# Optimization experiments

Measured on AMD Instinct MI355X. Metric: run time of the kernel, lower is better.

The kernel has to match this reference:

```python
import jax, jax.numpy as jnp
import numpy as np

ROT_DELTA = 1  # rotation_delta from __init__
BN_EPS = 1e-3  # keras BatchNormalization default epsilon


def conv_dirac(signal, bc_idx, bc_w, W, b):
    """Template-based intrinsic mesh conv (dirac patch operator).

    signal: [N, D]; bc_idx/bc_w: [N, Rr, A, 3]; W: [T, Rr, A, D]; b: [T].
    Returns [N, K, T] with K = A // ROT_DELTA rotations.
    """
    gathered = signal[bc_idx]  # [N, Rr, A, 3, D] irregular gather
    interp = jnp.einsum('vrai,vraid->vrad', bc_w, gathered)  # barycentric interp
    A = interp.shape[2]
    rots = np.arange(0, A, ROT_DELTA)
    # Rotating the (small) template weights is equivalent to rolling the
    # interpolated signal along the angular axis, but far cheaper.
    W_rot = jnp.stack([jnp.roll(W, int(r), axis=2) for r in rots])  # [K, T, Rr, A, D]
    return jnp.einsum('vrad,ktrad->vkt', interp, W_rot) + b  # [N, K, T]


def angular_max_pool(x):
    # Select, per vertex, the rotation whose response has maximal L2 norm.
    k = jnp.argmax(jnp.linalg.norm(x, axis=-1), axis=1)  # [N]
    return jnp.take_along_axis(x, k[:, None, None], axis=1)[:, 0]  # [N, T]


def batch_norm(x, gamma, beta):
    mu = jnp.mean(x, axis=0, keepdims=True)
    var = jnp.var(x, axis=0, keepdims=True)
    return gamma * (x - mu) * jax.lax.rsqrt(var + BN_EPS) + beta


def setup_inputs() -> dict:
    key = jax.random.key(0)
    ks = jax.random.split(key, 6)
    N, Rr, A, D, T = 80000, 5, 8, 32, 32
    signal = jax.random.normal(ks[0], (N, D), dtype=jnp.float32)
    bc_idx = jax.random.randint(ks[1], (N, Rr, A, 3), 0, N)
    bc_w = jax.random.uniform(ks[2], (N, Rr, A, 3), dtype=jnp.float32)
    bc_w = bc_w / jnp.sum(bc_w, axis=-1, keepdims=True)  # barycentric coords sum to 1
    W1 = jax.random.normal(ks[3], (T, Rr, A, D), dtype=jnp.float32) * 0.05
    W2 = jax.random.normal(ks[4], (T, Rr, A, D), dtype=jnp.float32) * 0.05
    return {
        'signal': signal, 'bc_idx': bc_idx, 'bc_w': bc_w,
        'W1': W1, 'b1': jnp.zeros((T,), jnp.float32),
        'gamma1': jnp.ones((T,), jnp.float32), 'beta1': jnp.zeros((T,), jnp.float32),
        'W2': W2, 'b2': jnp.zeros((T,), jnp.float32),
        'gamma2': jnp.ones((T,), jnp.float32), 'beta2': jnp.zeros((T,), jnp.float32),
    }


def reference(signal, bc_idx, bc_w, W1, b1, gamma1, beta1, W2, b2, gamma2, beta2):
    # Branch 1: conv -> angular max-pool -> BN -> relu
    s = conv_dirac(signal, bc_idx, bc_w, W1, b1)
    s = angular_max_pool(s)
    s = batch_norm(s, gamma1, beta1)
    s = jax.nn.relu(s)
    # Branch 2: conv -> angular max-pool -> BN
    s = conv_dirac(s, bc_idx, bc_w, W2, b2)
    s = angular_max_pool(s)
    s = batch_norm(s, gamma2, beta2)
    # Residual add (input_dim == amt_templates -> no rescale branch) + activation
    return jax.nn.relu(s + signal)
```

## Files before the change

kernel.cpp:

```cpp
#include <hip/hip_runtime.h>
#include <math.h>

#define RR 5
#define AA 8
#define DD 32
#define TT 32
#define KK 8

#define RT2 0.70710678118654752f

typedef float v2f __attribute__((ext_vector_type(2)));
typedef float v4f __attribute__((ext_vector_type(4)));

static __device__ __forceinline__ v2f pkfma(v2f a, v2f b, v2f c) {
#if __has_builtin(__builtin_elementwise_fma)
    return __builtin_elementwise_fma(a, b, c);
#else
    v2f r; r.x = fmaf(a.x, b.x, c.x); r.y = fmaf(a.y, b.y, c.y); return r;
#endif
}
static __device__ __forceinline__ v4f pkfma4(v4f a, v4f b, v4f c) {
#if __has_builtin(__builtin_elementwise_fma)
    return __builtin_elementwise_fma(a, b, c);
#else
    v4f r;
    r.x = fmaf(a.x, b.x, c.x); r.y = fmaf(a.y, b.y, c.y);
    r.z = fmaf(a.z, b.z, c.z); r.w = fmaf(a.w, b.w, c.w);
    return r;
#endif
}

__global__ void prep_kernel(const float* __restrict__ W1, const float* __restrict__ W2,
                            float* __restrict__ Ws1, float* __restrict__ Ws2,
                            double* __restrict__ dz, float* __restrict__ fz) {
    int b = blockIdx.x;
    int tid = threadIdx.x;
    if (b == 0 && tid < 128) { dz[tid] = 0.0; fz[tid] = 0.f; }
    int which = (b >= 20) ? 1 : 0;
    const float* __restrict__ W = which ? W2 : W1;
    float* __restrict__ Ws = which ? Ws2 : Ws1;
    int idx = (b - which * 20) * 256 + tid;
    if (idx >= TT * RR * DD) return;
    int d = idx & 31;
    int tr = idx >> 5;
    int t = tr / 5;
    int r = tr - t * 5;
    float xa[8];
    #pragma unroll
    for (int a = 0; a < 8; ++a) xa[a] = W[(tr * 8 + a) * 32 + d];
    float s0 = xa[0] + xa[4], d0 = xa[0] - xa[4];
    float s1 = xa[1] + xa[5], d1 = xa[1] - xa[5];
    float s2 = xa[2] + xa[6], d2 = xa[2] - xa[6];
    float s3 = xa[3] + xa[7], d3 = xa[3] - xa[7];
    float s02 = s0 + s2, s13 = s1 + s3;
    float F0 = s02 + s13, F4 = s02 - s13;
    float R2 = s0 - s2, I2 = s3 - s1;
    float u = RT2 * (d1 - d3), v = RT2 * (d1 + d3);
    float R1 = d0 + u, R3 = d0 - u;
    float I1 = -d2 - v, I3 = d2 - v;
    float* o = &Ws[(size_t)(r * 32 + d) * 256];
    *(v4f*)&o[t * 4]       = (v4f){F0, F4, R1, I1};
    *(v4f*)&o[128 + t * 4] = (v4f){R2, I2, R3, I3};
}

__global__ __launch_bounds__(256, 2)
void fused_conv_kernel(const float* __restrict__ sig,
                       const int* __restrict__ bc_idx,
                       const float* __restrict__ bc_w,
                       const float* __restrict__ Wsg,
                       const float* __restrict__ bias,
                       float* __restrict__ s_out,
                       double* __restrict__ sums,
                       double* __restrict__ sumsq,
                       int N) {
    __shared__ float Is[64 * 260];
    __shared__ float Wl[8 * 256];

    int tid = threadIdx.x;
    int vBase = blockIdx.x * 64;
    int lane = tid & 63;
    int wv = tid >> 6;

    int vg = lane & 7;
    int tg = lane >> 3;
    int v0L = wv * 16 + vg;
    int v1L = v0L + 8;
    int v0 = vBase + v0L;
    int v1 = vBase + v1L;

    int d4 = tid & 7;
    int g = tid >> 3;

    v2f A0[2][4], A1[2][4], A2[2][4], A3[2][4];
    #pragma unroll
    for (int vv = 0; vv < 2; ++vv)
        #pragma unroll
        for (int j = 0; j < 4; ++j) {
            A0[vv][j] = (v2f){0.f, 0.f}; A1[vv][j] = (v2f){0.f, 0.f};
            A2[vv][j] = (v2f){0.f, 0.f}; A3[vv][j] = (v2f){0.f, 0.f};
        }

    const v4f* Ws4 = (const v4f*)Wsg;

    for (int r = 0; r < RR; ++r) {
        __syncthreads();

        #pragma unroll
        for (int vv0 = 0; vv0 < 2; ++vv0) {
            int vv = g + vv0 * 32;
            int vgl = vBase + vv;
            int vgc = (vgl < N) ? vgl : (N - 1);
            int base = vgc * 120 + r * 24;
            int idxv[24]; float wbc[24];
            const int4* ib = (const int4*)(bc_idx + base);
            const float4* fb = (const float4*)(bc_w + base);
            #pragma unroll
            for (int q = 0; q < 6; ++q) {
                *(int4*)&idxv[q * 4] = ib[q];
                *(float4*)&wbc[q * 4] = fb[q];
            }
            v4f xa[8];
            #pragma unroll
            for (int a = 0; a < 8; ++a) {
                int i0 = idxv[a * 3 + 0];
                int i1 = idxv[a * 3 + 1];
                int i2 = idxv[a * 3 + 2];
                v4f r0 = *(const v4f*)&sig[(size_t)i0 * 32 + 4 * d4];
                v4f r1 = *(const v4f*)&sig[(size_t)i1 * 32 + 4 * d4];
                v4f r2 = *(const v4f*)&sig[(size_t)i2 * 32 + 4 * d4];
                float w0 = wbc[a * 3 + 0];
                float w1 = wbc[a * 3 + 1];
                float w2 = wbc[a * 3 + 2];
                v4f w0v = (v4f){w0, w0, w0, w0};
                v4f w1v = (v4f){w1, w1, w1, w1};
                v4f w2v = (v4f){w2, w2, w2, w2};
                xa[a] = pkfma4(w2v, r2, pkfma4(w1v, r1, w0v * r0));
            }
            v4f s0 = xa[0] + xa[4], dd0 = xa[0] - xa[4];
            v4f s1 = xa[1] + xa[5], dd1 = xa[1] - xa[5];
            v4f s2 = xa[2] + xa[6], dd2 = xa[2] - xa[6];
            v4f s3 = xa[3] + xa[7], dd3 = xa[3] - xa[7];
            v4f s02 = s0 + s2, s13 = s1 + s3;
            v4f F0 = s02 + s13, F4 = s02 - s13;
            v4f R2 = s0 - s2, I2 = s3 - s1;
            v4f u = RT2 * (dd1 - dd3), vt = RT2 * (dd1 + dd3);
            v4f R1 = dd0 + u, R3 = dd0 - u;
            v4f I1 = -dd2 - vt, I3 = dd2 - vt;
            float* ob = &Is[vv * 260 + d4 * 32];
            #pragma unroll
            for (int di = 0; di < 4; ++di) {
                *(v4f*)&ob[di * 8]     = (v4f){F0[di], F4[di], R1[di], I1[di]};
                *(v4f*)&ob[di * 8 + 4] = (v4f){R2[di], I2[di], R3[di], I3[di]};
            }
        }

        for (int ws = 0; ws < 4; ++ws) {
            __syncthreads();
            {
                const v4f* src = Ws4 + (size_t)(r * 32 + ws * 8) * 64;
                float* dst = &Wl[tid * 8];
                v4f a = src[tid * 2];
                v4f b = src[tid * 2 + 1];
                *(v4f*)dst = a;
                *(v4f*)(dst + 4) = b;
            }
            __syncthreads();

            #pragma unroll 2
            for (int dl = 0; dl < 8; ++dl) {
                const float* ip = &Is[v0L * 260 + (ws * 8 + dl) * 8];
                v4f pa0 = *(const v4f*)&ip[0];
                v4f pb0 = *(const v4f*)&ip[4];
                v4f pa1 = *(const v4f*)&ip[2080];
                v4f pb1 = *(const v4f*)&ip[2084];
                v2f x1_0 = pa0.zw, x1n_0 = {pa0.w, -pa0.z};
                v2f x2_0 = pb0.xy, x2n_0 = {pb0.y, -pb0.x};
                v2f x3_0 = pb0.zw, x3n_0 = {pb0.w, -pb0.z};
                v2f x1_1 = pa1.zw, x1n_1 = {pa1.w, -pa1.z};
                v2f x2_1 = pb1.xy, x2n_1 = {pb1.y, -pb1.x};
                v2f x3_1 = pb1.zw, x3n_1 = {pb1.w, -pb1.z};
                const float* wrow = &Wl[dl * 256];
                #pragma unroll
                for (int j = 0; j < 4; ++j) {
                    v4f q0 = *(const v4f*)&wrow[(tg + 8 * j) * 4];
                    v4f q1 = *(const v4f*)&wrow[(tg + 8 * j) * 4 + 128];
                    v2f w2v = {q0.z, q0.z}, w3v = {q0.w, q0.w};
                    v2f w4v = {q1.x, q1.x}, w5v = {q1.y, q1.y};
                    v2f w6v = {q1.z, q1.z}, w7v = {q1.w, q1.w};
                    A0[0][j] = pkfma(pa0.xy, q0.xy, A0[0][j]);
                    A1[0][j] = pkfma(x1_0, w2v, A1[0][j]);
                    A1[0][j] = pkfma(x1n_0, w3v, A1[0][j]);
                    A2[0][j] = pkfma(x2_0, w4v, A2[0][j]);
                    A2[0][j] = pkfma(x2n_0, w5v, A2[0][j]);
                    A3[0][j] = pkfma(x3_0, w6v, A3[0][j]);
                    A3[0][j] = pkfma(x3n_0, w7v, A3[0][j]);
                    A0[1][j] = pkfma(pa1.xy, q0.xy, A0[1][j]);
                    A1[1][j] = pkfma(x1_1, w2v, A1[1][j]);
                    A1[1][j] = pkfma(x1n_1, w3v, A1[1][j]);
                    A2[1][j] = pkfma(x2_1, w4v, A2[1][j]);
                    A2[1][j] = pkfma(x2n_1, w5v, A2[1][j]);
                    A3[1][j] = pkfma(x3_1, w6v, A3[1][j]);
                    A3[1][j] = pkfma(x3n_1, w7v, A3[1][j]);
                }
            }
        }
    }

    float bj[4];
    #pragma unroll
    for (int j = 0; j < 4; ++j) bj[j] = bias[tg + 8 * j];

    float outk[2][8][4];
    #pragma unroll
    for (int vv = 0; vv < 2; ++vv) {
        #pragma unroll
        for (int j = 0; j < 4; ++j) {
            float C0 = A0[vv][j].x, C4 = A0[vv][j].y;
            float R1 = A1[vv][j].x, I1 = A1[vv][j].y;
            float R2 = A2[vv][j].x, I2 = A2[vv][j].y;
            float R3 = A3[vv][j].x, I3 = A3[vv][j].y;
            float e = 0.125f * (C0 + C4), o = 0.125f * (C0 - C4);
            float p = 0.25f * (R1 + R3), q = 0.25f * R2, s = 0.25f * (I1 - I3);
            float a_ = 0.25f * RT2 * (R1 - R3);
            float b_ = 0.25f * RT2 * (I1 + I3);
            float c_ = 0.25f * I2;
            float bb = bj[j];
            outk[vv][0][j] = e + p + q + bb;
            outk[vv][1][j] = o + a_ - b_ - c_ + bb;
            outk[vv][2][j] = e - s - q + bb;
            outk[vv][3][j] = o - a_ - b_ + c_ + bb;
            outk[vv][4][j] = e - p + q + bb;
            outk[vv][5][j] = o - a_ + b_ - c_ + bb;
            outk[vv][6][j] = e + s - q + bb;
            outk[vv][7][j] = o + a_ + b_ + c_ + bb;
        }
    }

    float sel[2][4];
    int vOutA[2]; vOutA[0] = v0; vOutA[1] = v1;
    #pragma unroll
    for (int vv = 0; vv < 2; ++vv) {
        float norms[8];
        #pragma unroll
        for (int k = 0; k < 8; ++k) {
            float nl = 0.f;
            #pragma unroll
            for (int j = 0; j < 4; ++j)
                nl = fmaf(outk[vv][k][j], outk[vv][k][j], nl);
            nl += __shfl_xor(nl, 8);
            nl += __shfl_xor(nl, 16);
            nl += __shfl_xor(nl, 32);
            norms[k] = nl;
        }
        float best = -1.f;
        int bk = 0;
        #pragma unroll
        for (int k = 0; k < 8; ++k) {
            float n = sqrtf(norms[k]);
            if (n > best) { best = n; bk = k; }
        }
        #pragma unroll
        for (int j = 0; j < 4; ++j) sel[vv][j] = 0.f;
        #pragma unroll
        for (int k = 0; k < 8; ++k) {
            if (k == bk) {
                #pragma unroll
                for (int j = 0; j < 4; ++j) sel[vv][j] = outk[vv][k][j];
            }
        }
        if (vOutA[vv] < N) {
            float* o = s_out + (size_t)vOutA[vv] * 32 + tg;
            o[0]  = sel[vv][0];
            o[8]  = sel[vv][1];
            o[16] = sel[vv][2];
            o[24] = sel[vv][3];
        }
    }

    float pa_[4], pb_[4];
    #pragma unroll
    for (int j = 0; j < 4; ++j) {
        float s0 = (v0 < N) ? sel[0][j] : 0.f;
        float s1 = (v1 < N) ? sel[1][j] : 0.f;
        pa_[j] = s0 + s1;
        pb_[j] = fmaf(s0, s0, s1 * s1);
    }
    #pragma unroll
    for (int j = 0; j < 4; ++j) {
        pa_[j] += __shfl_xor(pa_[j], 1);
        pb_[j] += __shfl_xor(pb_[j], 1);
        pa_[j] += __shfl_xor(pa_[j], 2);
        pb_[j] += __shfl_xor(pb_[j], 2);
        pa_[j] += __shfl_xor(pa_[j], 4);
        pb_[j] += __shfl_xor(pb_[j], 4);
    }
    __syncthreads();
    if (vg == 0) {
        float* wst = (float*)Wl;
        #pragma unroll
        for (int j = 0; j < 4; ++j) {
            int t = tg + 8 * j;
            wst[(wv * 32 + t) * 2 + 0] = pa_[j];
            wst[(wv * 32 + t) * 2 + 1] = pb_[j];
        }
    }
    __syncthreads();
    if (tid < 64) {
        const float* wst = (const float*)Wl;
        int t = tid >> 1, c = tid & 1;
        float s = wst[t * 2 + c] + wst[64 + t * 2 + c] +
                  wst[128 + t * 2 + c] + wst[192 + t * 2 + c];
        if (c == 0) atomicAdd(&sums[t], (double)s);
        else        atomicAdd(&sumsq[t], (double)s);
    }
}

__global__ void finalize_kernel(const double* __restrict__ sums,
                                const double* __restrict__ sumsq,
                                const float* __restrict__ gamma,
                                const float* __restrict__ beta,
                                float* __restrict__ scale,
                                float* __restrict__ shift, int n) {
    int t = threadIdx.x;
    if (t < 32) {
        double mu = sums[t] / (double)n;
        double var = sumsq[t] / (double)n - mu * mu;
        double sc = (double)gamma[t] / sqrt(var + 1e-3);
        scale[t] = (float)sc;
        shift[t] = (float)((double)beta[t] - mu * sc);
    }
}

__global__ void affine_relu_kernel(const float* __restrict__ s,
                                   const float* __restrict__ scale,
                                   const float* __restrict__ shift,
                                   float* __restrict__ o, int n4) {
    int e = blockIdx.x * blockDim.x + threadIdx.x;
    if (e >= n4) return;
    int t0 = (e & 7) * 4;
    float4 x = ((const float4*)s)[e];
    float4 y;
    y.x = fmaxf(fmaf(scale[t0 + 0], x.x, shift[t0 + 0]), 0.f);
    y.y = fmaxf(fmaf(scale[t0 + 1], x.y, shift[t0 + 1]), 0.f);
    y.z = fmaxf(fmaf(scale[t0 + 2], x.z, shift[t0 + 2]), 0.f);
    y.w = fmaxf(fmaf(scale[t0 + 3], x.w, shift[t0 + 3]), 0.f);
    ((float4*)o)[e] = y;
}

__global__ void final_kernel(const float* __restrict__ s,
                             const float* __restrict__ scale,
                             const float* __restrict__ shift,
                             const float* __restrict__ sig,
                             float* __restrict__ o, int n4) {
    int e = blockIdx.x * blockDim.x + threadIdx.x;
    if (e >= n4) return;
    int t0 = (e & 7) * 4;
    float4 x = ((const float4*)s)[e];
    float4 z = ((const float4*)sig)[e];
    float4 y;
    y.x = fmaxf(fmaf(scale[t0 + 0], x.x, shift[t0 + 0]) + z.x, 0.f);
    y.y = fmaxf(fmaf(scale[t0 + 1], x.y, shift[t0 + 1]) + z.y, 0.f);
    y.z = fmaxf(fmaf(scale[t0 + 2], x.z, shift[t0 + 2]) + z.z, 0.f);
    y.w = fmaxf(fmaf(scale[t0 + 3], x.w, shift[t0 + 3]) + z.w, 0.f);
    ((float4*)o)[e] = y;
}

extern "C" void kernel_launch(void* const* d_in, const int* in_sizes, int n_in,
                              void* d_out, int out_size, void* d_ws, size_t ws_size,
                              hipStream_t stream) {
    const float* signal = (const float*)d_in[0];
    const int* bc_idx   = (const int*)d_in[1];
    const float* bc_w   = (const float*)d_in[2];
    const float* W1     = (const float*)d_in[3];
    const float* b1     = (const float*)d_in[4];
    const float* g1     = (const float*)d_in[5];
    const float* be1    = (const float*)d_in[6];
    const float* W2     = (const float*)d_in[7];
    const float* b2     = (const float*)d_in[8];
    const float* g2     = (const float*)d_in[9];
    const float* be2    = (const float*)d_in[10];
    float* out = (float*)d_out;

    const int N = in_sizes[0] / 32;

    char* ws = (char*)d_ws;
    double* sums1  = (double*)ws;
    double* sumsq1 = sums1 + 32;
    double* sums2  = sums1 + 64;
    double* sumsq2 = sums1 + 96;
    float* scale1 = (float*)(ws + 1024);
    float* shift1 = scale1 + 32;
    float* scale2 = scale1 + 64;
    float* shift2 = scale1 + 96;
    float* Ws1 = (float*)(ws + 4096);
    float* Ws2 = Ws1 + RR * DD * TT * 8;
    float* s1  = Ws2 + RR * DD * TT * 8;
    float* sg2 = s1 + (size_t)N * 32;
    float* s2  = sg2 + (size_t)N * 32;

    int nBlocks = (N + 63) / 64;

    prep_kernel<<<40, 256, 0, stream>>>(W1, W2, Ws1, Ws2, (double*)ws, (float*)(ws + 1024));

    fused_conv_kernel<<<nBlocks, 256, 0, stream>>>(signal, bc_idx, bc_w, Ws1, b1, s1,
                                                   sums1, sumsq1, N);
    finalize_kernel<<<1, 32, 0, stream>>>(sums1, sumsq1, g1, be1, scale1, shift1, N);
    affine_relu_kernel<<<(N * 8 + 255) / 256, 256, 0, stream>>>(s1, scale1, shift1, sg2, N * 8);

    fused_conv_kernel<<<nBlocks, 256, 0, stream>>>(sg2, bc_idx, bc_w, Ws2, b2, s2,
                                                   sums2, sumsq2, N);
    finalize_kernel<<<1, 32, 0, stream>>>(sums2, sumsq2, g2, be2, scale2, shift2, N);

    final_kernel<<<(N * 8 + 255) / 256, 256, 0, stream>>>(s2, scale2, shift2, signal, out, N * 8);
}
```

Measured before the change: 627.4 us.

## Remap conv threads so each wave owns eight templates with wave-uniform scalar weight loads

```diff
diff --git a/kernel.cpp b/kernel.cpp
--- a/kernel.cpp
+++ b/kernel.cpp
@@ -18,6 +18,10 @@
 #else
     v2f r; r.x = fmaf(a.x, b.x, c.x); r.y = fmaf(a.y, b.y, c.y); return r;
 #endif
+}
+static __device__ __forceinline__ v2f pkfmas(v2f a, float s, v2f c) {
+    v2f b = {s, s};
+    return pkfma(a, b, c);
 }
 static __device__ __forceinline__ v4f pkfma4(v4f a, v4f b, v4f c) {
 #if __has_builtin(__builtin_elementwise_fma)
@@ -58,9 +62,10 @@
     float u = RT2 * (d1 - d3), v = RT2 * (d1 + d3);
     float R1 = d0 + u, R3 = d0 - u;
     float I1 = -d2 - v, I3 = d2 - v;
-    float* o = &Ws[(size_t)(r * 32 + d) * 256];
-    *(v4f*)&o[t * 4]       = (v4f){F0, F4, R1, I1};
-    *(v4f*)&o[128 + t * 4] = (v4f){R2, I2, R3, I3};
+    int wq = t >> 3, tq = t & 7;
+    float* o = &Ws[(size_t)((((r * 32 + d) * 4 + wq) * 64) + tq * 8)];
+    *(v4f*)&o[0] = (v4f){F0, F4, R1, I1};
+    *(v4f*)&o[4] = (v4f){R2, I2, R3, I3};
 }
 
 __global__ __launch_bounds__(256, 2)
@@ -74,33 +79,26 @@
                        double* __restrict__ sumsq,
                        int N) {
     __shared__ float Is[64 * 260];
-    __shared__ float Wl[8 * 256];
+    __shared__ float NrmS[4 * 64 * 8];
 
     int tid = threadIdx.x;
     int vBase = blockIdx.x * 64;
     int lane = tid & 63;
     int wv = tid >> 6;
-
-    int vg = lane & 7;
-    int tg = lane >> 3;
-    int v0L = wv * 16 + vg;
-    int v1L = v0L + 8;
-    int v0 = vBase + v0L;
-    int v1 = vBase + v1L;
+    int wvu = __builtin_amdgcn_readfirstlane(wv);
 
     int d4 = tid & 7;
     int g = tid >> 3;
 
-    v2f A0[2][4], A1[2][4], A2[2][4], A3[2][4];
-    #pragma unroll
-    for (int vv = 0; vv < 2; ++vv)
-        #pragma unroll
-        for (int j = 0; j < 4; ++j) {
-            A0[vv][j] = (v2f){0.f, 0.f}; A1[vv][j] = (v2f){0.f, 0.f};
-            A2[vv][j] = (v2f){0.f, 0.f}; A3[vv][j] = (v2f){0.f, 0.f};
-        }
-
-    const v4f* Ws4 = (const v4f*)Wsg;
+    int vL = lane;
+    int v = vBase + vL;
+
+    v2f A0[8], A1[8], A2[8], A3[8];
+    #pragma unroll
+    for (int tq = 0; tq < 8; ++tq) {
+        A0[tq] = (v2f){0.f, 0.f}; A1[tq] = (v2f){0.f, 0.f};
+        A2[tq] = (v2f){0.f, 0.f}; A3[tq] = (v2f){0.f, 0.f};
+    }
 
     for (int r = 0; r < RR; ++r) {
         __syncthreads();
@@ -153,165 +151,120 @@
                 *(v4f*)&ob[di * 8 + 4] = (v4f){R2[di], I2[di], R3[di], I3[di]};
             }
         }
-
-        for (int ws = 0; ws < 4; ++ws) {
-            __syncthreads();
-            {
-                const v4f* src = Ws4 + (size_t)(r * 32 + ws * 8) * 64;
-                float* dst = &Wl[tid * 8];
-                v4f a = src[tid * 2];
-                v4f b = src[tid * 2 + 1];
-                *(v4f*)dst = a;
-                *(v4f*)(dst + 4) = b;
-            }
-            __syncthreads();
-
-            #pragma unroll 2
-            for (int dl = 0; dl < 8; ++dl) {
-                const float* ip = &Is[v0L * 260 + (ws * 8 + dl) * 8];
-                v4f pa0 = *(const v4f*)&ip[0];
-                v4f pb0 = *(const v4f*)&ip[4];
-                v4f pa1 = *(const v4f*)&ip[2080];
-                v4f pb1 = *(const v4f*)&ip[2084];
-                v2f x1_0 = pa0.zw, x1n_0 = {pa0.w, -pa0.z};
-                v2f x2_0 = pb0.xy, x2n_0 = {pb0.y, -pb0.x};
-                v2f x3_0 = pb0.zw, x3n_0 = {pb0.w, -pb0.z};
-                v2f x1_1 = pa1.zw, x1n_1 = {pa1.w, -pa1.z};
-                v2f x2_1 = pb1.xy, x2n_1 = {pb1.y, -pb1.x};
-                v2f x3_1 = pb1.zw, x3n_1 = {pb1.w, -pb1.z};
-                const float* wrow = &Wl[dl * 256];
-                #pragma unroll
-                for (int j = 0; j < 4; ++j) {
-                    v4f q0 = *(const v4f*)&wrow[(tg + 8 * j) * 4];
-                    v4f q1 = *(const v4f*)&wrow[(tg + 8 * j) * 4 + 128];
-                    v2f w2v = {q0.z, q0.z}, w3v = {q0.w, q0.w};
-                    v2f w4v = {q1.x, q1.x}, w5v = {q1.y, q1.y};
-                    v2f w6v = {q1.z, q1.z}, w7v = {q1.w, q1.w};
-                    A0[0][j] = pkfma(pa0.xy, q0.xy, A0[0][j]);
-                    A1[0][j] = pkfma(x1_0, w2v, A1[0][j]);
-                    A1[0][j] = pkfma(x1n_0, w3v, A1[0][j]);
-                    A2[0][j] = pkfma(x2_0, w4v, A2[0][j]);
-                    A2[0][j] = pkfma(x2n_0, w5v, A2[0][j]);
-                    A3[0][j] = pkfma(x3_0, w6v, A3[0][j]);
-                    A3[0][j] = pkfma(x3n_0, w7v, A3[0][j]);
-                    A0[1][j] = pkfma(pa1.xy, q0.xy, A0[1][j]);
-                    A1[1][j] = pkfma(x1_1, w2v, A1[1][j]);
-                    A1[1][j] = pkfma(x1n_1, w3v, A1[1][j]);
-                    A2[1][j] = pkfma(x2_1, w4v, A2[1][j]);
-                    A2[1][j] = pkfma(x2n_1, w5v, A2[1][j]);
-                    A3[1][j] = pkfma(x3_1, w6v, A3[1][j]);
-                    A3[1][j] = pkfma(x3n_1, w7v, A3[1][j]);
-                }
+        __syncthreads();
+
+        const float* ip0 = &Is[vL * 260];
+        #pragma unroll 2
+        for (int dl = 0; dl < 32; ++dl) {
+            v4f pa = *(const v4f*)&ip0[dl * 8];
+            v4f pb = *(const v4f*)&ip0[dl * 8 + 4];
+            v2f x1 = pa.zw, x1n = {pa.w, -pa.z};
+            v2f x2 = pb.xy, x2n = {pb.y, -pb.x};
+            v2f x3 = pb.zw, x3n = {pb.w, -pb.z};
+            const float* wb = &Wsg[(size_t)(((r * 32 + dl) * 4 + wvu) * 64)];
+            #pragma unroll
+            for (int tq = 0; tq < 8; ++tq) {
+                v2f q01 = {wb[tq * 8 + 0], wb[tq * 8 + 1]};
+                float q0z = wb[tq * 8 + 2], q0w = wb[tq * 8 + 3];
+                float q1x = wb[tq * 8 + 4], q1y = wb[tq * 8 + 5];
+                float q1z = wb[tq * 8 + 6], q1w = wb[tq * 8 + 7];
+                A0[tq] = pkfma(pa.xy, q01, A0[tq]);
+                A1[tq] = pkfmas(x1, q0z, A1[tq]);
+                A1[tq] = pkfmas(x1n, q0w, A1[tq]);
+                A2[tq] = pkfmas(x2, q1x, A2[tq]);
+                A2[tq] = pkfmas(x2n, q1y, A2[tq]);
+                A3[tq] = pkfmas(x3, q1z, A3[tq]);
+                A3[tq] = pkfmas(x3n, q1w, A3[tq]);
             }
         }
     }
 
-    float bj[4];
-    #pragma unroll
-    for (int j = 0; j < 4; ++j) bj[j] = bias[tg + 8 * j];
-
-    float outk[2][8][4];
-    #pragma unroll
-    for (int vv = 0; vv < 2; ++vv) {
-        #pragma unroll
-        for (int j = 0; j < 4; ++j) {
-            float C0 = A0[vv][j].x, C4 = A0[vv][j].y;
-            float R1 = A1[vv][j].x, I1 = A1[vv][j].y;
-            float R2 = A2[vv][j].x, I2 = A2[vv][j].y;
-            float R3 = A3[vv][j].x, I3 = A3[vv][j].y;
-            float e = 0.125f * (C0 + C4), o = 0.125f * (C0 - C4);
-            float p = 0.25f * (R1 + R3), q = 0.25f * R2, s = 0.25f * (I1 - I3);
-            float a_ = 0.25f * RT2 * (R1 - R3);
-            float b_ = 0.25f * RT2 * (I1 + I3);
-            float c_ = 0.25f * I2;
-            float bb = bj[j];
-            outk[vv][0][j] = e + p + q + bb;
-            outk[vv][1][j] = o + a_ - b_ - c_ + bb;
-            outk[vv][2][j] = e - s - q + bb;
-            outk[vv][3][j] = o - a_ - b_ + c_ + bb;
-            outk[vv][4][j] = e - p + q + bb;
-            outk[vv][5][j] = o - a_ + b_ - c_ + bb;
-            outk[vv][6][j] = e + s - q + bb;
-            outk[vv][7][j] = o + a_ + b_ + c_ + bb;
+    float nrm[8];
+    #pragma unroll
+    for (int k = 0; k < 8; ++k) nrm[k] = 0.f;
+
+    float outk[8][8];
+    #pragma unroll
+    for (int tq = 0; tq < 8; ++tq) {
+        float bb = bias[wvu * 8 + tq];
+        float C0 = A0[tq].x, C4 = A0[tq].y;
+        float R1 = A1[tq].x, I1 = A1[tq].y;
+        float R2 = A2[tq].x, I2 = A2[tq].y;
+        float R3 = A3[tq].x, I3 = A3[tq].y;
+        float e = 0.125f * (C0 + C4), o = 0.125f * (C0 - C4);
+        float p = 0.25f * (R1 + R3), q = 0.25f * R2, s = 0.25f * (I1 - I3);
+        float a_ = 0.25f * RT2 * (R1 - R3);
+        float b_ = 0.25f * RT2 * (I1 + I3);
+        float c_ = 0.25f * I2;
+        outk[tq][0] = e + p + q + bb;
+        outk[tq][1] = o + a_ - b_ - c_ + bb;
+        outk[tq][2] = e - s - q + bb;
+        outk[tq][3] = o - a_ - b_ + c_ + bb;
+        outk[tq][4] = e - p + q + bb;
+        outk[tq][5] = o - a_ + b_ - c_ + bb;
+        outk[tq][6] = e + s - q + bb;
+        outk[tq][7] = o + a_ + b_ + c_ + bb;
+        #pragma unroll
+        for (int k = 0; k < 8; ++k)
+            nrm[k] = fmaf(outk[tq][k], outk[tq][k], nrm[k]);
+    }
+
+    {
+        float* nb = &NrmS[(wvu * 64 + vL) * 8];
+        *(v4f*)&nb[0] = (v4f){nrm[0], nrm[1], nrm[2], nrm[3]};
+        *(v4f*)&nb[4] = (v4f){nrm[4], nrm[5], nrm[6], nrm[7]};
+    }
+    __syncthreads();
+    v4f t0 = {0.f, 0.f, 0.f, 0.f}, t1 = {0.f, 0.f, 0.f, 0.f};
+    #pragma unroll
+    for (int w = 0; w < 4; ++w) {
+        const float* nb = &NrmS[(w * 64 + vL) * 8];
+        t0 += *(const v4f*)&nb[0];
+        t1 += *(const v4f*)&nb[4];
+    }
+    float tot[8] = {t0.x, t0.y, t0.z, t0.w, t1.x, t1.y, t1.z, t1.w};
+    int bk = 0;
+    float best = tot[0];
+    #pragma unroll
+    for (int k = 1; k < 8; ++k) {
+        if (tot[k] > best) { best = tot[k]; bk = k; }
+    }
+
+    float selv[8];
+    #pragma unroll
+    for (int tq = 0; tq < 8; ++tq) {
+        float sv = outk[tq][0];
+        #pragma unroll
+        for (int k = 1; k < 8; ++k) sv = (bk == k) ? outk[tq][k] : sv;
+        selv[tq] = sv;
+    }
+    if (v < N) {
+        float* o = s_out + (size_t)v * 32 + wvu * 8;
+        *(v4f*)&o[0] = (v4f){selv[0], selv[1], selv[2], selv[3]};
+        *(v4f*)&o[4] = (v4f){selv[4], selv[5], selv[6], selv[7]};
+    }
+
+    float sa[8], sb[8];
+    #pragma unroll
+    for (int tq = 0; tq < 8; ++tq) {
+        float x = (v < N) ? selv[tq] : 0.f;
+        sa[tq] = x;
+        sb[tq] = x * x;
+    }
+    #pragma unroll
+    for (int off = 1; off < 64; off <<= 1) {
+        #pragma unroll
+        for (int tq = 0; tq < 8; ++tq) {
+            sa[tq] += __shfl_xor(sa[tq], off);
+            sb[tq] += __shfl_xor(sb[tq], off);
         }
     }
-
-    float sel[2][4];
-    int vOutA[2]; vOutA[0] = v0; vOutA[1] = v1;
-    #pragma unroll
-    for (int vv = 0; vv < 2; ++vv) {
-        float norms[8];
-        #pragma unroll
-        for (int k = 0; k < 8; ++k) {
-            float nl = 0.f;
-            #pragma unroll
-            for (int j = 0; j < 4; ++j)
-                nl = fmaf(outk[vv][k][j], outk[vv][k][j], nl);
-            nl += __shfl_xor(nl, 8);
-            nl += __shfl_xor(nl, 16);
-            nl += __shfl_xor(nl, 32);
-            norms[k] = nl;
+    if (lane == 0) {
+        #pragma unroll
+        for (int tq = 0; tq < 8; ++tq) {
+            atomicAdd(&sums[wvu * 8 + tq], (double)sa[tq]);
+            atomicAdd(&sumsq[wvu * 8 + tq], (double)sb[tq]);
         }
-        float best = -1.f;
-        int bk = 0;
-        #pragma unroll
-        for (int k = 0; k < 8; ++k) {
-            float n = sqrtf(norms[k]);
-            if (n > best) { best = n; bk = k; }
-        }
-        #pragma unroll
-        for (int j = 0; j < 4; ++j) sel[vv][j] = 0.f;
-        #pragma unroll
-        for (int k = 0; k < 8; ++k) {
-            if (k == bk) {
-                #pragma unroll
-                for (int j = 0; j < 4; ++j) sel[vv][j] = outk[vv][k][j];
-            }
-        }
-        if (vOutA[vv] < N) {
-            float* o = s_out + (size_t)vOutA[vv] * 32 + tg;
-            o[0]  = sel[vv][0];
-            o[8]  = sel[vv][1];
-            o[16] = sel[vv][2];
-            o[24] = sel[vv][3];
-        }
-    }
-
-    float pa_[4], pb_[4];
-    #pragma unroll
-    for (int j = 0; j < 4; ++j) {
-        float s0 = (v0 < N) ? sel[0][j] : 0.f;
-        float s1 = (v1 < N) ? sel[1][j] : 0.f;
-        pa_[j] = s0 + s1;
-        pb_[j] = fmaf(s0, s0, s1 * s1);
-    }
-    #pragma unroll
-    for (int j = 0; j < 4; ++j) {
-        pa_[j] += __shfl_xor(pa_[j], 1);
-        pb_[j] += __shfl_xor(pb_[j], 1);
-        pa_[j] += __shfl_xor(pa_[j], 2);
-        pb_[j] += __shfl_xor(pb_[j], 2);
-        pa_[j] += __shfl_xor(pa_[j], 4);
-        pb_[j] += __shfl_xor(pb_[j], 4);
-    }
-    __syncthreads();
-    if (vg == 0) {
-        float* wst = (float*)Wl;
-        #pragma unroll
-        for (int j = 0; j < 4; ++j) {
-            int t = tg + 8 * j;
-            wst[(wv * 32 + t) * 2 + 0] = pa_[j];
-            wst[(wv * 32 + t) * 2 + 1] = pb_[j];
-        }
-    }
-    __syncthreads();
-    if (tid < 64) {
-        const float* wst = (const float*)Wl;
-        int t = tid >> 1, c = tid & 1;
-        float s = wst[t * 2 + c] + wst[64 + t * 2 + c] +
-                  wst[128 + t * 2 + c] + wst[192 + t * 2 + c];
-        if (c == 0) atomicAdd(&sums[t], (double)s);
-        else        atomicAdd(&sumsq[t], (double)s);
     }
 }
 
```

Result: slower. 1.053 ms (+67.8%).

## Retile conv GEMM to 4 vertices x 4 templates per thread with D-split halves

Applied to the files above, without the earlier changes.

```diff
diff --git a/kernel.cpp b/kernel.cpp
--- a/kernel.cpp
+++ b/kernel.cpp
@@ -58,9 +58,9 @@
     float u = RT2 * (d1 - d3), v = RT2 * (d1 + d3);
     float R1 = d0 + u, R3 = d0 - u;
     float I1 = -d2 - v, I3 = d2 - v;
-    float* o = &Ws[(size_t)(r * 32 + d) * 256];
-    *(v4f*)&o[t * 4]       = (v4f){F0, F4, R1, I1};
-    *(v4f*)&o[128 + t * 4] = (v4f){R2, I2, R3, I3};
+    float* o = &Ws[(size_t)((r * 32 + d) * 256 + t * 8)];
+    o[0] = F0; o[1] = F4; o[2] = R1; o[3] = I1;
+    o[4] = R2; o[5] = I2; o[6] = R3; o[7] = I3;
 }
 
 __global__ __launch_bounds__(256, 2)
@@ -74,33 +74,29 @@
                        double* __restrict__ sumsq,
                        int N) {
     __shared__ float Is[64 * 260];
-    __shared__ float Wl[8 * 256];
+    __shared__ float Wl[2304];
 
     int tid = threadIdx.x;
     int vBase = blockIdx.x * 64;
     int lane = tid & 63;
     int wv = tid >> 6;
 
-    int vg = lane & 7;
-    int tg = lane >> 3;
-    int v0L = wv * 16 + vg;
-    int v1L = v0L + 8;
-    int v0 = vBase + v0L;
-    int v1 = vBase + v1L;
+    int vg = lane & 3;
+    int tg = (lane >> 2) & 7;
+    int dh = lane >> 5;
+    int vbL = wv * 16 + vg * 4;
 
     int d4 = tid & 7;
     int g = tid >> 3;
 
-    v2f A0[2][4], A1[2][4], A2[2][4], A3[2][4];
-    #pragma unroll
-    for (int vv = 0; vv < 2; ++vv)
+    v2f A0[4][4], A1[4][4], A2[4][4], A3[4][4];
+    #pragma unroll
+    for (int vv = 0; vv < 4; ++vv)
         #pragma unroll
         for (int j = 0; j < 4; ++j) {
             A0[vv][j] = (v2f){0.f, 0.f}; A1[vv][j] = (v2f){0.f, 0.f};
             A2[vv][j] = (v2f){0.f, 0.f}; A3[vv][j] = (v2f){0.f, 0.f};
         }
-
-    const v4f* Ws4 = (const v4f*)Wsg;
 
     for (int r = 0; r < RR; ++r) {
         __syncthreads();
@@ -143,10 +139,10 @@
             v4f s02 = s0 + s2, s13 = s1 + s3;
             v4f F0 = s02 + s13, F4 = s02 - s13;
             v4f R2 = s0 - s2, I2 = s3 - s1;
-            v4f u = RT2 * (dd1 - dd3), vt = RT2 * (dd1 + dd3);
+            v4f u = RT2 * (dd1 - dd3), vt_ = RT2 * (dd1 + dd3);
             v4f R1 = dd0 + u, R3 = dd0 - u;
-            v4f I1 = -dd2 - vt, I3 = dd2 - vt;
-            float* ob = &Is[vv * 260 + d4 * 32];
+            v4f I1 = -dd2 - vt_, I3 = dd2 - vt_;
+            float* ob = &Is[vv * 260 + d4 * 32 + (d4 >> 2) * 4];
             #pragma unroll
             for (int di = 0; di < 4; ++di) {
                 *(v4f*)&ob[di * 8]     = (v4f){F0[di], F4[di], R1[di], I1[di]};
@@ -157,62 +153,78 @@
         for (int ws = 0; ws < 4; ++ws) {
             __syncthreads();
             {
-                const v4f* src = Ws4 + (size_t)(r * 32 + ws * 8) * 64;
-                float* dst = &Wl[tid * 8];
-                v4f a = src[tid * 2];
-                v4f b = src[tid * 2 + 1];
-                *(v4f*)dst = a;
-                *(v4f*)(dst + 4) = b;
+                int row = tid >> 5;
+                int rem = tid & 31;
+                int stg = rem >> 2;
+                int sjj = rem & 3;
+                int d = (row < 4) ? (ws * 4 + row) : (12 + ws * 4 + row);
+                const float* src = &Wsg[(size_t)((r * 32 + d) * 256 + (stg * 4 + sjj) * 8)];
+                float* dst = &Wl[row * 288 + stg * 36 + sjj * 8];
+                v4f a = *(const v4f*)&src[0];
+                v4f b = *(const v4f*)&src[4];
+                *(v4f*)&dst[0] = a;
+                *(v4f*)&dst[4] = b;
             }
             __syncthreads();
 
-            #pragma unroll 2
-            for (int dl = 0; dl < 8; ++dl) {
-                const float* ip = &Is[v0L * 260 + (ws * 8 + dl) * 8];
-                v4f pa0 = *(const v4f*)&ip[0];
-                v4f pb0 = *(const v4f*)&ip[4];
-                v4f pa1 = *(const v4f*)&ip[2080];
-                v4f pb1 = *(const v4f*)&ip[2084];
-                v2f x1_0 = pa0.zw, x1n_0 = {pa0.w, -pa0.z};
-                v2f x2_0 = pb0.xy, x2n_0 = {pb0.y, -pb0.x};
-                v2f x3_0 = pb0.zw, x3n_0 = {pb0.w, -pb0.z};
-                v2f x1_1 = pa1.zw, x1n_1 = {pa1.w, -pa1.z};
-                v2f x2_1 = pb1.xy, x2n_1 = {pb1.y, -pb1.x};
-                v2f x3_1 = pb1.zw, x3n_1 = {pb1.w, -pb1.z};
-                const float* wrow = &Wl[dl * 256];
+            #pragma unroll
+            for (int dli = 0; dli < 4; ++dli) {
+                int dgl = dh * 16 + ws * 4 + dli;
+                int icol = dgl * 8 + dh * 4;
+                const float* wr = &Wl[(dh * 4 + dli) * 288 + tg * 36];
+                v4f q0[4], q1[4];
                 #pragma unroll
                 for (int j = 0; j < 4; ++j) {
-                    v4f q0 = *(const v4f*)&wrow[(tg + 8 * j) * 4];
-                    v4f q1 = *(const v4f*)&wrow[(tg + 8 * j) * 4 + 128];
-                    v2f w2v = {q0.z, q0.z}, w3v = {q0.w, q0.w};
-                    v2f w4v = {q1.x, q1.x}, w5v = {q1.y, q1.y};
-                    v2f w6v = {q1.z, q1.z}, w7v = {q1.w, q1.w};
-                    A0[0][j] = pkfma(pa0.xy, q0.xy, A0[0][j]);
-                    A1[0][j] = pkfma(x1_0, w2v, A1[0][j]);
-                    A1[0][j] = pkfma(x1n_0, w3v, A1[0][j]);
-                    A2[0][j] = pkfma(x2_0, w4v, A2[0][j]);
-                    A2[0][j] = pkfma(x2n_0, w5v, A2[0][j]);
-                    A3[0][j] = pkfma(x3_0, w6v, A3[0][j]);
-                    A3[0][j] = pkfma(x3n_0, w7v, A3[0][j]);
-                    A0[1][j] = pkfma(pa1.xy, q0.xy, A0[1][j]);
-                    A1[1][j] = pkfma(x1_1, w2v, A1[1][j]);
-                    A1[1][j] = pkfma(x1n_1, w3v, A1[1][j]);
-                    A2[1][j] = pkfma(x2_1, w4v, A2[1][j]);
-                    A2[1][j] = pkfma(x2n_1, w5v, A2[1][j]);
-                    A3[1][j] = pkfma(x3_1, w6v, A3[1][j]);
-                    A3[1][j] = pkfma(x3n_1, w7v, A3[1][j]);
+                    q0[j] = *(const v4f*)&wr[j * 8];
+                    q1[j] = *(const v4f*)&wr[j * 8 + 4];
                 }
-            }
-        }
-    }
+                #pragma unroll
+                for (int vv = 0; vv < 4; ++vv) {
+                    const float* ip = &Is[(vbL + vv) * 260 + icol];
+                    v4f pa = *(const v4f*)&ip[0];
+                    v4f pb = *(const v4f*)&ip[4];
+                    v2f x1 = pa.zw, x1n = {pa.w, -pa.z};
+                    v2f x2 = pb.xy, x2n = {pb.y, -pb.x};
+                    v2f x3 = pb.zw, x3n = {pb.w, -pb.z};
+                    #pragma unroll
+                    for (int j = 0; j < 4; ++j) {
+                        v2f w2v = {q0[j].z, q0[j].z}, w3v = {q0[j].w, q0[j].w};
+                        v2f w4v = {q1[j].x, q1[j].x}, w5v = {q1[j].y, q1[j].y};
+                        v2f w6v = {q1[j].z, q1[j].z}, w7v = {q1[j].w, q1[j].w};
+                        A0[vv][j] = pkfma(pa.xy, q0[j].xy, A0[vv][j]);
+                        A1[vv][j] = pkfma(x1, w2v, A1[vv][j]);
+                        A1[vv][j] = pkfma(x1n, w3v, A1[vv][j]);
+                        A2[vv][j] = pkfma(x2, w4v, A2[vv][j]);
+                        A2[vv][j] = pkfma(x2n, w5v, A2[vv][j]);
+                        A3[vv][j] = pkfma(x3, w6v, A3[vv][j]);
+                        A3[vv][j] = pkfma(x3n, w7v, A3[vv][j]);
+                    }
+                }
+            }
+        }
+    }
+
+    #pragma unroll
+    for (int vv = 0; vv < 4; ++vv)
+        #pragma unroll
+        for (int j = 0; j < 4; ++j) {
+            A0[vv][j].x += __shfl_xor(A0[vv][j].x, 32);
+            A0[vv][j].y += __shfl_xor(A0[vv][j].y, 32);
+            A1[vv][j].x += __shfl_xor(A1[vv][j].x, 32);
+            A1[vv][j].y += __shfl_xor(A1[vv][j].y, 32);
+            A2[vv][j].x += __shfl_xor(A2[vv][j].x, 32);
+            A2[vv][j].y += __shfl_xor(A2[vv][j].y, 32);
+            A3[vv][j].x += __shfl_xor(A3[vv][j].x, 32);
+            A3[vv][j].y += __shfl_xor(A3[vv][j].y, 32);
+        }
 
     float bj[4];
     #pragma unroll
-    for (int j = 0; j < 4; ++j) bj[j] = bias[tg + 8 * j];
-
-    float outk[2][8][4];
-    #pragma unroll
-    for (int vv = 0; vv < 2; ++vv) {
+    for (int j = 0; j < 4; ++j) bj[j] = bias[tg * 4 + j];
+
+    float outL[4][4][4];
+    #pragma unroll
+    for (int vv = 0; vv < 4; ++vv) {
         #pragma unroll
         for (int j = 0; j < 4; ++j) {
             float C0 = A0[vv][j].x, C4 = A0[vv][j].y;
@@ -225,83 +237,94 @@
             float b_ = 0.25f * RT2 * (I1 + I3);
             float c_ = 0.25f * I2;
             float bb = bj[j];
-            outk[vv][0][j] = e + p + q + bb;
-            outk[vv][1][j] = o + a_ - b_ - c_ + bb;
-            outk[vv][2][j] = e - s - q + bb;
-            outk[vv][3][j] = o - a_ - b_ + c_ + bb;
-            outk[vv][4][j] = e - p + q + bb;
-            outk[vv][5][j] = o - a_ + b_ - c_ + bb;
-            outk[vv][6][j] = e + s - q + bb;
-            outk[vv][7][j] = o + a_ + b_ + c_ + bb;
-        }
-    }
-
-    float sel[2][4];
-    int vOutA[2]; vOutA[0] = v0; vOutA[1] = v1;
-    #pragma unroll
-    for (int vv = 0; vv < 2; ++vv) {
-        float norms[8];
-        #pragma unroll
-        for (int k = 0; k < 8; ++k) {
+            float o0 = e + p + q + bb, o4 = e - p + q + bb;
+            float o1 = o + a_ - b_ - c_ + bb, o5 = o - a_ + b_ - c_ + bb;
+            float o2 = e - s - q + bb, o6 = e + s - q + bb;
+            float o3 = o - a_ - b_ + c_ + bb, o7 = o + a_ + b_ + c_ + bb;
+            outL[vv][0][j] = dh ? o4 : o0;
+            outL[vv][1][j] = dh ? o5 : o1;
+            outL[vv][2][j] = dh ? o6 : o2;
+            outL[vv][3][j] = dh ? o7 : o3;
+        }
+    }
+
+    float nrm[4][4], pn[4][4];
+    #pragma unroll
+    for (int vv = 0; vv < 4; ++vv)
+        #pragma unroll
+        for (int kk = 0; kk < 4; ++kk) {
             float nl = 0.f;
             #pragma unroll
             for (int j = 0; j < 4; ++j)
-                nl = fmaf(outk[vv][k][j], outk[vv][k][j], nl);
+                nl = fmaf(outL[vv][kk][j], outL[vv][kk][j], nl);
+            nl += __shfl_xor(nl, 4);
             nl += __shfl_xor(nl, 8);
             nl += __shfl_xor(nl, 16);
-            nl += __shfl_xor(nl, 32);
-            norms[k] = nl;
-        }
-        float best = -1.f;
+            nrm[vv][kk] = nl;
+            pn[vv][kk] = __shfl_xor(nl, 32);
+        }
+
+    float sa[4] = {0.f, 0.f, 0.f, 0.f};
+    float sb[4] = {0.f, 0.f, 0.f, 0.f};
+
+    #pragma unroll
+    for (int vv = 0; vv < 4; ++vv) {
+        float n8[8];
+        #pragma unroll
+        for (int kk = 0; kk < 4; ++kk) {
+            float a = nrm[vv][kk], b = pn[vv][kk];
+            n8[kk]     = dh ? b : a;
+            n8[kk + 4] = dh ? a : b;
+        }
         int bk = 0;
-        #pragma unroll
-        for (int k = 0; k < 8; ++k) {
-            float n = sqrtf(norms[k]);
-            if (n > best) { best = n; bk = k; }
-        }
-        #pragma unroll
-        for (int j = 0; j < 4; ++j) sel[vv][j] = 0.f;
-        #pragma unroll
-        for (int k = 0; k < 8; ++k) {
-            if (k == bk) {
+        float best = n8[0];
+        #pragma unroll
+        for (int k = 1; k < 8; ++k) {
+            if (n8[k] > best) { best = n8[k]; bk = k; }
+        }
+        int winhere = ((bk >> 2) == dh);
+        int bkk = bk & 3;
+        float sv[4] = {0.f, 0.f, 0.f, 0.f};
+        #pragma unroll
+        for (int kk = 0; kk < 4; ++kk) {
+            if (kk == bkk) {
                 #pragma unroll
-                for (int j = 0; j < 4; ++j) sel[vv][j] = outk[vv][k][j];
-            }
-        }
-        if (vOutA[vv] < N) {
-            float* o = s_out + (size_t)vOutA[vv] * 32 + tg;
-            o[0]  = sel[vv][0];
-            o[8]  = sel[vv][1];
-            o[16] = sel[vv][2];
-            o[24] = sel[vv][3];
-        }
-    }
-
-    float pa_[4], pb_[4];
+                for (int j = 0; j < 4; ++j) sv[j] = outL[vv][kk][j];
+            }
+        }
+        #pragma unroll
+        for (int j = 0; j < 4; ++j) {
+            sv[j] = winhere ? sv[j] : 0.f;
+            sv[j] += __shfl_xor(sv[j], 32);
+        }
+        int v = vBase + vbL + vv;
+        if (dh == 0 && v < N) {
+            *(v4f*)&s_out[(size_t)v * 32 + tg * 4] = (v4f){sv[0], sv[1], sv[2], sv[3]};
+        }
+        float msk = (v < N) ? 1.f : 0.f;
+        #pragma unroll
+        for (int j = 0; j < 4; ++j) {
+            float x = msk * sv[j];
+            sa[j] += x;
+            sb[j] = fmaf(x, x, sb[j]);
+        }
+    }
+
     #pragma unroll
     for (int j = 0; j < 4; ++j) {
-        float s0 = (v0 < N) ? sel[0][j] : 0.f;
-        float s1 = (v1 < N) ? sel[1][j] : 0.f;
-        pa_[j] = s0 + s1;
-        pb_[j] = fmaf(s0, s0, s1 * s1);
-    }
-    #pragma unroll
-    for (int j = 0; j < 4; ++j) {
-        pa_[j] += __shfl_xor(pa_[j], 1);
-        pb_[j] += __shfl_xor(pb_[j], 1);
-        pa_[j] += __shfl_xor(pa_[j], 2);
-        pb_[j] += __shfl_xor(pb_[j], 2);
-        pa_[j] += __shfl_xor(pa_[j], 4);
-        pb_[j] += __shfl_xor(pb_[j], 4);
+        sa[j] += __shfl_xor(sa[j], 1);
+        sb[j] += __shfl_xor(sb[j], 1);
+        sa[j] += __shfl_xor(sa[j], 2);
+        sb[j] += __shfl_xor(sb[j], 2);
     }
     __syncthreads();
-    if (vg == 0) {
+    if (dh == 0 && vg == 0) {
         float* wst = (float*)Wl;
         #pragma unroll
         for (int j = 0; j < 4; ++j) {
-            int t = tg + 8 * j;
-            wst[(wv * 32 + t) * 2 + 0] = pa_[j];
-            wst[(wv * 32 + t) * 2 + 1] = pb_[j];
+            int t = tg * 4 + j;
+            wst[(wv * 32 + t) * 2 + 0] = sa[j];
+            wst[(wv * 32 + t) * 2 + 1] = sb[j];
         }
     }
     __syncthreads();
```

Result: slower. 733.1 us (+16.9%).

## Make each wave own its vertices and read weights directly from global memory

Applied to the files above, without the earlier changes.

```diff
diff --git a/kernel.cpp b/kernel.cpp
--- a/kernel.cpp
+++ b/kernel.cpp
@@ -58,9 +58,9 @@
     float u = RT2 * (d1 - d3), v = RT2 * (d1 + d3);
     float R1 = d0 + u, R3 = d0 - u;
     float I1 = -d2 - v, I3 = d2 - v;
-    float* o = &Ws[(size_t)(r * 32 + d) * 256];
-    *(v4f*)&o[t * 4]       = (v4f){F0, F4, R1, I1};
-    *(v4f*)&o[128 + t * 4] = (v4f){R2, I2, R3, I3};
+    float* o = &Ws[(size_t)((r * 32 + d) * 256 + t * 8)];
+    o[0] = F0; o[1] = F4; o[2] = R1; o[3] = I1;
+    o[4] = R2; o[5] = I2; o[6] = R3; o[7] = I3;
 }
 
 __global__ __launch_bounds__(256, 2)
@@ -74,7 +74,7 @@
                        double* __restrict__ sumsq,
                        int N) {
     __shared__ float Is[64 * 260];
-    __shared__ float Wl[8 * 256];
+    __shared__ float StS[256];
 
     int tid = threadIdx.x;
     int vBase = blockIdx.x * 64;
@@ -88,8 +88,8 @@
     int v0 = vBase + v0L;
     int v1 = vBase + v1L;
 
-    int d4 = tid & 7;
-    int g = tid >> 3;
+    int d4 = lane & 7;
+    int g8 = lane >> 3;
 
     v2f A0[2][4], A1[2][4], A2[2][4], A3[2][4];
     #pragma unroll
@@ -100,15 +100,11 @@
             A2[vv][j] = (v2f){0.f, 0.f}; A3[vv][j] = (v2f){0.f, 0.f};
         }
 
-    const v4f* Ws4 = (const v4f*)Wsg;
-
     for (int r = 0; r < RR; ++r) {
-        __syncthreads();
-
         #pragma unroll
         for (int vv0 = 0; vv0 < 2; ++vv0) {
-            int vv = g + vv0 * 32;
-            int vgl = vBase + vv;
+            int vvL = wv * 16 + vv0 * 8 + g8;
+            int vgl = vBase + vvL;
             int vgc = (vgl < N) ? vgl : (N - 1);
             int base = vgc * 120 + r * 24;
             int idxv[24]; float wbc[24];
@@ -143,67 +139,59 @@
             v4f s02 = s0 + s2, s13 = s1 + s3;
             v4f F0 = s02 + s13, F4 = s02 - s13;
             v4f R2 = s0 - s2, I2 = s3 - s1;
-            v4f u = RT2 * (dd1 - dd3), vt = RT2 * (dd1 + dd3);
+            v4f u = RT2 * (dd1 - dd3), vt_ = RT2 * (dd1 + dd3);
             v4f R1 = dd0 + u, R3 = dd0 - u;
-            v4f I1 = -dd2 - vt, I3 = dd2 - vt;
-            float* ob = &Is[vv * 260 + d4 * 32];
+            v4f I1 = -dd2 - vt_, I3 = dd2 - vt_;
+            float* ob = &Is[vvL * 260 + d4 * 32 + (d4 >> 2) * 4];
             #pragma unroll
             for (int di = 0; di < 4; ++di) {
                 *(v4f*)&ob[di * 8]     = (v4f){F0[di], F4[di], R1[di], I1[di]};
                 *(v4f*)&ob[di * 8 + 4] = (v4f){R2[di], I2[di], R3[di], I3[di]};
             }
         }
-
-        for (int ws = 0; ws < 4; ++ws) {
-            __syncthreads();
-            {
-                const v4f* src = Ws4 + (size_t)(r * 32 + ws * 8) * 64;
-                float* dst = &Wl[tid * 8];
-                v4f a = src[tid * 2];
-                v4f b = src[tid * 2 + 1];
-                *(v4f*)dst = a;
-                *(v4f*)(dst + 4) = b;
+        asm volatile("s_waitcnt lgkmcnt(0)" ::: "memory");
+        __builtin_amdgcn_sched_barrier(0);
+
+        const float* wrb = &Wsg[(size_t)(r * 32) * 256];
+        #pragma unroll 2
+        for (int dl = 0; dl < 32; ++dl) {
+            const float* ip = &Is[v0L * 260 + dl * 8 + (dl >> 4) * 4];
+            v4f pa0 = *(const v4f*)&ip[0];
+            v4f pb0 = *(const v4f*)&ip[4];
+            v4f pa1 = *(const v4f*)&ip[2080];
+            v4f pb1 = *(const v4f*)&ip[2084];
+            v2f x1_0 = pa0.zw, x1n_0 = {pa0.w, -pa0.z};
+            v2f x2_0 = pb0.xy, x2n_0 = {pb0.y, -pb0.x};
+            v2f x3_0 = pb0.zw, x3n_0 = {pb0.w, -pb0.z};
+            v2f x1_1 = pa1.zw, x1n_1 = {pa1.w, -pa1.z};
+            v2f x2_1 = pb1.xy, x2n_1 = {pb1.y, -pb1.x};
+            v2f x3_1 = pb1.zw, x3n_1 = {pb1.w, -pb1.z};
+            const float* wrow = wrb + dl * 256;
+            #pragma unroll
+            for (int j = 0; j < 4; ++j) {
+                v4f q0 = *(const v4f*)&wrow[(tg + 8 * j) * 8];
+                v4f q1 = *(const v4f*)&wrow[(tg + 8 * j) * 8 + 4];
+                v2f w2v = {q0.z, q0.z}, w3v = {q0.w, q0.w};
+                v2f w4v = {q1.x, q1.x}, w5v = {q1.y, q1.y};
+                v2f w6v = {q1.z, q1.z}, w7v = {q1.w, q1.w};
+                A0[0][j] = pkfma(pa0.xy, q0.xy, A0[0][j]);
+                A1[0][j] = pkfma(x1_0, w2v, A1[0][j]);
+                A1[0][j] = pkfma(x1n_0, w3v, A1[0][j]);
+                A2[0][j] = pkfma(x2_0, w4v, A2[0][j]);
+                A2[0][j] = pkfma(x2n_0, w5v, A2[0][j]);
+                A3[0][j] = pkfma(x3_0, w6v, A3[0][j]);
+                A3[0][j] = pkfma(x3n_0, w7v, A3[0][j]);
+                A0[1][j] = pkfma(pa1.xy, q0.xy, A0[1][j]);
+                A1[1][j] = pkfma(x1_1, w2v, A1[1][j]);
+                A1[1][j] = pkfma(x1n_1, w3v, A1[1][j]);
+                A2[1][j] = pkfma(x2_1, w4v, A2[1][j]);
+                A2[1][j] = pkfma(x2n_1, w5v, A2[1][j]);
+                A3[1][j] = pkfma(x3_1, w6v, A3[1][j]);
+                A3[1][j] = pkfma(x3n_1, w7v, A3[1][j]);
             }
-            __syncthreads();
-
-            #pragma unroll 2
-            for (int dl = 0; dl < 8; ++dl) {
-                const float* ip = &Is[v0L * 260 + (ws * 8 + dl) * 8];
-                v4f pa0 = *(const v4f*)&ip[0];
-                v4f pb0 = *(const v4f*)&ip[4];
-                v4f pa1 = *(const v4f*)&ip[2080];
-                v4f pb1 = *(const v4f*)&ip[2084];
-                v2f x1_0 = pa0.zw, x1n_0 = {pa0.w, -pa0.z};
-                v2f x2_0 = pb0.xy, x2n_0 = {pb0.y, -pb0.x};
-                v2f x3_0 = pb0.zw, x3n_0 = {pb0.w, -pb0.z};
-                v2f x1_1 = pa1.zw, x1n_1 = {pa1.w, -pa1.z};
-                v2f x2_1 = pb1.xy, x2n_1 = {pb1.y, -pb1.x};
-                v2f x3_1 = pb1.zw, x3n_1 = {pb1.w, -pb1.z};
-                const float* wrow = &Wl[dl * 256];
-                #pragma unroll
-                for (int j = 0; j < 4; ++j) {
-                    v4f q0 = *(const v4f*)&wrow[(tg + 8 * j) * 4];
-                    v4f q1 = *(const v4f*)&wrow[(tg + 8 * j) * 4 + 128];
-                    v2f w2v = {q0.z, q0.z}, w3v = {q0.w, q0.w};
-                    v2f w4v = {q1.x, q1.x}, w5v = {q1.y, q1.y};
-                    v2f w6v = {q1.z, q1.z}, w7v = {q1.w, q1.w};
-                    A0[0][j] = pkfma(pa0.xy, q0.xy, A0[0][j]);
-                    A1[0][j] = pkfma(x1_0, w2v, A1[0][j]);
-                    A1[0][j] = pkfma(x1n_0, w3v, A1[0][j]);
-                    A2[0][j] = pkfma(x2_0, w4v, A2[0][j]);
-                    A2[0][j] = pkfma(x2n_0, w5v, A2[0][j]);
-                    A3[0][j] = pkfma(x3_0, w6v, A3[0][j]);
-                    A3[0][j] = pkfma(x3n_0, w7v, A3[0][j]);
-                    A0[1][j] = pkfma(pa1.xy, q0.xy, A0[1][j]);
-                    A1[1][j] = pkfma(x1_1, w2v, A1[1][j]);
-                    A1[1][j] = pkfma(x1n_1, w3v, A1[1][j]);
-                    A2[1][j] = pkfma(x2_1, w4v, A2[1][j]);
-                    A2[1][j] = pkfma(x2n_1, w5v, A2[1][j]);
-                    A3[1][j] = pkfma(x3_1, w6v, A3[1][j]);
-                    A3[1][j] = pkfma(x3n_1, w7v, A3[1][j]);
-                }
-            }
-        }
+        }
+        asm volatile("s_waitcnt lgkmcnt(0)" ::: "memory");
+        __builtin_amdgcn_sched_barrier(0);
     }
 
     float bj[4];
@@ -296,20 +284,18 @@
     }
     __syncthreads();
     if (vg == 0) {
-        float* wst = (float*)Wl;
         #pragma unroll
         for (int j = 0; j < 4; ++j) {
             int t = tg + 8 * j;
-            wst[(wv * 32 + t) * 2 + 0] = pa_[j];
-            wst[(wv * 32 + t) * 2 + 1] = pb_[j];
+            StS[(wv * 32 + t) * 2 + 0] = pa_[j];
+            StS[(wv * 32 + t) * 2 + 1] = pb_[j];
         }
     }
     __syncthreads();
     if (tid < 64) {
-        const float* wst = (const float*)Wl;
         int t = tid >> 1, c = tid & 1;
-        float s = wst[t * 2 + c] + wst[64 + t * 2 + c] +
-                  wst[128 + t * 2 + c] + wst[192 + t * 2 + c];
+        float s = StS[t * 2 + c] + StS[64 + t * 2 + c] +
+                  StS[128 + t * 2 + c] + StS[192 + t * 2 + c];
         if (c == 0) atomicAdd(&sums[t], (double)s);
         else        atomicAdd(&sumsq[t], (double)s);
     }
```

Result: slower. 678.4 us (+8.1%).
